# Kernel tuning notes

Hardware: AMD Instinct MI355X
Metric: run time of the kernel (lower is better)

## Reference

```python
import jax, jax.numpy as jnp
import numpy as np

ALPHA = 0.15  # top-k fraction (forward default)


def setup_inputs() -> dict:
    key = jax.random.key(0)
    k1, k2, k3 = jax.random.split(key, 3)
    B, N, D = 8, 1024, 256
    x = jax.random.normal(k1, (B, N, D), dtype=jnp.float32)
    # torch nn.Linear(dim, H*head_dim, bias=False); stored here as [D, H*head_dim]
    W_src = jax.random.normal(k2, (D, D), dtype=jnp.float32) * (1.0 / np.sqrt(D))
    W_tgt = jax.random.normal(k3, (D, D), dtype=jnp.float32) * (1.0 / np.sqrt(D))
    return {"x": x, "W_src": W_src, "W_tgt": W_tgt}


def _topk_mask(adj, k):
    # adj: [B,H,N,N]; exact scatter of 1.0 at top-k indices along last axis
    B, H, N, _ = adj.shape
    _, idx = jax.lax.top_k(adj, k)              # [B,H,N,k]
    bi = jnp.arange(B)[:, None, None, None]
    hi = jnp.arange(H)[None, :, None, None]
    ni = jnp.arange(N)[None, None, :, None]
    mask = jnp.zeros_like(adj).at[bi, hi, ni, idx].set(1.0)
    return mask


def reference(x, W_src, W_tgt):
    # directed=True path of DirectedGraphLearner.forward
    B, N, D = x.shape
    H, head_dim = 4, D // 4
    k = max(1, int(ALPHA * N))
    src = (x @ W_src).reshape(B, N, H, head_dim)
    tgt = (x @ W_tgt).reshape(B, N, H, head_dim)
    adj = jnp.einsum('bihd,bjhd->bhij', src, tgt)
    adj = jax.nn.gelu(adj, approximate=False)    # torch F.gelu default = exact erf
    mask = _topk_mask(adj, k)
    return adj * mask
```

## Files before the change

kernel.cpp:

```cpp
#include <hip/hip_runtime.h>
#include <math.h>


#define KSEL 153u
#define EPSK 61000u

typedef __attribute__((ext_vector_type(8))) short short8v;
typedef __attribute__((ext_vector_type(4))) float float4v;

__device__ __forceinline__ float gelu_f32(float x) {
    return 0.5f * x * (1.0f + erff(x * 0.70710678118654752f));
}

__device__ __forceinline__ unsigned long long d2key(double v) {
    unsigned long long u = (unsigned long long)__double_as_longlong(v);
    return (u >> 63) ? ~u : (u | 0x8000000000000000ull);
}

__device__ __forceinline__ unsigned lkeyf(float v) {
    float q = fmaf(v, 33554432.0f, 2147483648.0f);
    q = fminf(fmaxf(q, 0.0f), 4294967040.0f);
    return (unsigned)q;
}

__device__ __forceinline__ unsigned short b16(float x) {
    unsigned u = __float_as_uint(x);
    u += 0x7FFFu + ((u >> 16) & 1u);
    return (unsigned short)(u >> 16);
}
__device__ __forceinline__ float bf2f(unsigned short h) {
    return __uint_as_float(((unsigned)h) << 16);
}
__device__ __forceinline__ unsigned pk2(float a, float b) {
    return (unsigned)b16(a) | ((unsigned)b16(b) << 16);
}

#define LGKM0()                                             \
    do {                                                    \
        asm volatile("s_waitcnt lgkmcnt(0)" ::: "memory");  \
        __builtin_amdgcn_sched_barrier(0);                  \
    } while (0)

template <bool W32>
__global__ __launch_bounds__(256) void k1_proj(const float* __restrict__ x,
                                               const float* __restrict__ Wsrc,
                                               const float* __restrict__ Wtgt,
                                               double* __restrict__ ws,
                                               unsigned short* __restrict__ th,
                                               unsigned short* __restrict__ tl) {
    __shared__ float xs[32 * 68];
    __shared__ float wsh[32 * 68];
    const int t = threadIdx.x;
    const int bx = blockIdx.x;
    const int by = blockIdx.y;
    const int col0 = (by & 3) * 64;
    const float* __restrict__ W = (by < 4) ? Wsrc : Wtgt;
    double* __restrict__ outp = ws + ((by < 4) ? 0 : 2097152);

    double acc[4][4];
#pragma unroll
    for (int i = 0; i < 4; ++i)
#pragma unroll
        for (int j = 0; j < 4; ++j) acc[i][j] = 0.0;

    const int m_loc = (t & 15) * 4;
    const int c_loc = (t >> 4) * 4;

    for (int kt = 0; kt < 8; ++kt) {
        __syncthreads();
#pragma unroll
        for (int it = 0; it < 2; ++it) {
            int f4 = t + 256 * it;
            int m = f4 >> 3, k4 = f4 & 7;
            float4 v = *reinterpret_cast<const float4*>(&x[(bx * 64 + m) * 256 + kt * 32 + 4 * k4]);
            xs[(4 * k4 + 0) * 68 + m] = v.x;
            xs[(4 * k4 + 1) * 68 + m] = v.y;
            xs[(4 * k4 + 2) * 68 + m] = v.z;
            xs[(4 * k4 + 3) * 68 + m] = v.w;
        }
#pragma unroll
        for (int it = 0; it < 2; ++it) {
            int f4 = t + 256 * it;
            int k = f4 >> 4, c4 = f4 & 15;
            *reinterpret_cast<float4*>(&wsh[k * 68 + 4 * c4]) =
                *reinterpret_cast<const float4*>(&W[(kt * 32 + k) * 256 + col0 + 4 * c4]);
        }
        __syncthreads();
#pragma unroll
        for (int kk = 0; kk < 32; ++kk) {
            float4 a = *reinterpret_cast<const float4*>(&xs[kk * 68 + m_loc]);
            float4 b = *reinterpret_cast<const float4*>(&wsh[kk * 68 + c_loc]);
            double ad[4] = {a.x, a.y, a.z, a.w};
            double bd[4] = {b.x, b.y, b.z, b.w};
#pragma unroll
            for (int i = 0; i < 4; ++i)
#pragma unroll
                for (int j = 0; j < 4; ++j) acc[i][j] += ad[i] * bd[j];
        }
    }
    const int hd = by & 3;
#pragma unroll
    for (int i = 0; i < 4; ++i) {
        int m = bx * 64 + m_loc + i;
        int b = m >> 10, n = m & 1023;
        int bhd = b * 4 + hd;
        size_t base = ((size_t)(bhd * 1024 + n)) * 64 + c_loc;
        double2 v01, v23;
        v01.x = acc[i][0]; v01.y = acc[i][1];
        v23.x = acc[i][2]; v23.y = acc[i][3];
        *reinterpret_cast<double2*>(&outp[base]) = v01;
        *reinterpret_cast<double2*>(&outp[base + 2]) = v23;
        if (W32 && by >= 4) {
            float f0 = (float)acc[i][0], f1 = (float)acc[i][1];
            float f2 = (float)acc[i][2], f3 = (float)acc[i][3];
            unsigned short h0 = b16(f0), h1 = b16(f1), h2 = b16(f2), h3 = b16(f3);
            uint2 H, L;
            H.x = (unsigned)h0 | ((unsigned)h1 << 16);
            H.y = (unsigned)h2 | ((unsigned)h3 << 16);
            L.x = pk2(f0 - bf2f(h0), f1 - bf2f(h1));
            L.y = pk2(f2 - bf2f(h2), f3 - bf2f(h3));
            *reinterpret_cast<uint2*>(&th[base]) = H;
            *reinterpret_cast<uint2*>(&tl[base]) = L;
        }
    }
}

template <bool FAST>
__global__ __launch_bounds__(256, 4) void k2_fused(const double* __restrict__ srcT,
                                                   const double* __restrict__ tgtT,
                                                   const unsigned short* __restrict__ th,
                                                   const unsigned short* __restrict__ tlo,
                                                   float* __restrict__ out) {
    __shared__ float tr[16 * 512];
    __shared__ unsigned short srcf[2][1024];
    __shared__ __align__(16) unsigned hist[4][256];

    const int t = threadIdx.x;
    const int lane = t & 63;
    const int wv = t >> 6;
    const int bid = (blockIdx.x & 7) * 256 + (blockIdx.x >> 3);
    const int bh = bid >> 6;
    const int itile = bid & 63;
    const int row0 = itile * 16;
    const int r0 = 4 * wv;
    const size_t tgtBase = (size_t)bh * 65536;
    const unsigned short* __restrict__ thb = th + tgtBase;
    const unsigned short* __restrict__ tlb = tlo + tgtBase;

    {
        int r = t >> 4, dq = (t & 15) * 4;
        const double* sp = &srcT[((size_t)bh * 1024 + row0 + r) * 64 + dq];
        double2 a = *reinterpret_cast<const double2*>(sp);
        double2 b = *reinterpret_cast<const double2*>(sp + 2);
        float f0 = (float)a.x, f1 = (float)a.y, f2 = (float)b.x, f3 = (float)b.y;
        unsigned short h0 = b16(f0), h1 = b16(f1), h2 = b16(f2), h3 = b16(f3);
        int s = dq >> 3;
        int idx = r * 64 + ((s ^ (r & 7)) << 3) + (dq & 7);
        uint2 H, L;
        H.x = (unsigned)h0 | ((unsigned)h1 << 16);
        H.y = (unsigned)h2 | ((unsigned)h3 << 16);
        L.x = pk2(f0 - bf2f(h0), f1 - bf2f(h1));
        L.y = pk2(f2 - bf2f(h2), f3 - bf2f(h3));
        *reinterpret_cast<uint2*>(&srcf[0][idx]) = H;
        *reinterpret_cast<uint2*>(&srcf[1][idx]) = L;
    }
    __syncthreads();

    short8v Ah[2], Al[2];
#pragma unroll
    for (int ks = 0; ks < 2; ++ks) {
        int idxA = (lane & 15) * 64 + (((4 * ks + (lane >> 4)) ^ (lane & 7)) << 3);
        Ah[ks] = *reinterpret_cast<const short8v*>(&srcf[0][idxA]);
        Al[ks] = *reinterpret_cast<const short8v*>(&srcf[1][idxA]);
    }

    const int colA = lane & 15;
    const int kgrp = lane >> 4;
    float vals[4][16];

#pragma unroll
    for (int h = 0; h < 2; ++h) {
        float4v acc[8];
#pragma unroll
        for (int a = 0; a < 8; ++a) acc[a] = (float4v){0.f, 0.f, 0.f, 0.f};

#pragma unroll
        for (int u = 0; u < 8; ++u) {
            const int T = 32 * h + 4 * u + wv;
            const size_t cbase = (size_t)(16 * T + colA) * 64 + kgrp * 8;
#pragma unroll
            for (int ks = 0; ks < 2; ++ks) {
                short8v Bh, Bl;
                if (FAST) {
                    Bh = *reinterpret_cast<const short8v*>(&thb[cbase + 32 * ks]);
                    Bl = *reinterpret_cast<const short8v*>(&tlb[cbase + 32 * ks]);
                } else {
                    const double* gp = &tgtT[tgtBase + cbase + 32 * ks];
                    double2 d0 = *reinterpret_cast<const double2*>(gp);
                    double2 d1 = *reinterpret_cast<const double2*>(gp + 2);
                    double2 d2 = *reinterpret_cast<const double2*>(gp + 4);
                    double2 d3 = *reinterpret_cast<const double2*>(gp + 6);
                    float f[8] = {(float)d0.x, (float)d0.y, (float)d1.x, (float)d1.y,
                                  (float)d2.x, (float)d2.y, (float)d3.x, (float)d3.y};
                    unsigned short hh[8];
#pragma unroll
                    for (int e = 0; e < 8; ++e) hh[e] = b16(f[e]);
                    unsigned Hw[4], Lw[4];
#pragma unroll
                    for (int e = 0; e < 4; ++e) {
                        Hw[e] = (unsigned)hh[2 * e] | ((unsigned)hh[2 * e + 1] << 16);
                        Lw[e] = pk2(f[2 * e] - bf2f(hh[2 * e]), f[2 * e + 1] - bf2f(hh[2 * e + 1]));
                    }
                    Bh = *reinterpret_cast<const short8v*>(Hw);
                    Bl = *reinterpret_cast<const short8v*>(Lw);
                }
                acc[u] = __builtin_amdgcn_mfma_f32_16x16x32_bf16(Ah[ks], Bh, acc[u], 0, 0, 0);
                acc[u] = __builtin_amdgcn_mfma_f32_16x16x32_bf16(Al[ks], Bh, acc[u], 0, 0, 0);
                acc[u] = __builtin_amdgcn_mfma_f32_16x16x32_bf16(Ah[ks], Bl, acc[u], 0, 0, 0);
            }
        }

        __syncthreads();
#pragma unroll
        for (int u = 0; u < 8; ++u) {
            int colh = 16 * (4 * u + wv) + colA;
#pragma unroll
            for (int reg = 0; reg < 4; ++reg) {
                int row = 4 * kgrp + reg;
                tr[row * 512 + (colh ^ ((row & 1) << 4))] = acc[u][reg];
            }
        }
        __syncthreads();
#pragma unroll
        for (int ri = 0; ri < 4; ++ri) {
            int row = r0 + ri;
#pragma unroll
            for (int mm = 0; mm < 8; ++mm) {
                int colh = lane + 64 * mm;
                vals[ri][8 * h + mm] = tr[row * 512 + (colh ^ ((row & 1) << 4))];
            }
        }
    }

    const size_t outBase = ((size_t)bh * 1024 + row0 + r0) * 1024;
    unsigned* cjp = &hist[wv][128];
    unsigned long long* ckp = reinterpret_cast<unsigned long long*>(&hist[wv][0]);
    unsigned* ccp = &hist[wv][192];

#pragma unroll
    for (int ri = 0; ri < 4; ++ri) {
        unsigned ul[16];
#pragma unroll
        for (int m = 0; m < 16; ++m) ul[m] = lkeyf(vals[ri][m]);

        unsigned prefA = 0u, maskA = 0u, rk = KSEL;
#pragma unroll 1
        for (int p = 1; p >= 0; --p) {
            const int sh = 16 + 8 * p;
            *reinterpret_cast<uint4*>(&hist[wv][4 * lane]) = make_uint4(0u, 0u, 0u, 0u);
            LGKM0();
#pragma unroll
            for (int m = 0; m < 16; ++m) {
                if ((ul[m] & maskA) == prefA)
                    atomicAdd(&hist[wv][(ul[m] >> sh) & 255u], 1u);
            }
            LGKM0();
            unsigned h0 = hist[wv][4 * lane + 0], h1 = hist[wv][4 * lane + 1];
            unsigned h2 = hist[wv][4 * lane + 2], h3 = hist[wv][4 * lane + 3];
            unsigned S = h0 + h1 + h2 + h3;
            unsigned inc = S;
#pragma unroll
            for (int off = 1; off < 64; off <<= 1) {
                unsigned o = __shfl_down(inc, off, 64);
                inc = (lane + off < 64) ? (inc + o) : inc;
            }
            unsigned above = inc - S;
            bool found = (above < rk) && (rk <= inc);
            unsigned long long bal = __ballot(found);
            int L = __ffsll(bal) - 1;
            unsigned hh[4];
            hh[0] = __shfl(h0, L, 64);
            hh[1] = __shfl(h1, L, 64);
            hh[2] = __shfl(h2, L, 64);
            hh[3] = __shfl(h3, L, 64);
            unsigned cum = __shfl(above, L, 64);
            int bsel = -1;
#pragma unroll
            for (int q = 3; q >= 0; --q) {
                if (bsel < 0) {
                    if (rk <= cum + hh[q]) {
                        bsel = q;
                        rk = rk - cum;
                    } else {
                        cum += hh[q];
                    }
                }
            }
            prefA |= (unsigned)(4 * L + bsel) << sh;
            maskA |= 0xFFu << sh;
        }

        const unsigned klo = prefA - EPSK;
        const unsigned khi = prefA + 65535u + EPSK;

        int ch = 0, cb = 0;
#pragma unroll
        for (int m = 0; m < 16; ++m) {
            ch += (ul[m] > khi) ? 1 : 0;
            cb += (ul[m] >= klo && ul[m] <= khi) ? 1 : 0;
        }
#pragma unroll
        for (int off = 32; off; off >>= 1) {
            ch += __shfl_xor(ch, off, 64);
            cb += __shfl_xor(cb, off, 64);
        }
        const unsigned need = KSEL - (unsigned)ch;
        const bool fastp = ((unsigned)cb == need);

        unsigned long long selMask = 0ull;
        unsigned cidx[16];
        if (!fastp) {
            if (lane == 0) *ccp = 0u;
            LGKM0();
#pragma unroll
            for (int m = 0; m < 16; ++m) {
                cidx[m] = 0xFFFFFFFFu;
                if (ul[m] >= klo && ul[m] <= khi) {
                    unsigned idx = atomicAdd(ccp, 1u);
                    cidx[m] = idx;
                    if (idx < 64u) cjp[idx] = (unsigned)(lane + 64 * m);
                }
            }
            LGKM0();
            unsigned g = *ccp;
            if (g > 64u) g = 64u;
            unsigned rnk = need;
            if (lane < (int)g) {
                unsigned j = cjp[lane];
                const double2* sp = reinterpret_cast<const double2*>(
                    &srcT[((size_t)bh * 1024 + row0 + r0 + ri) * 64]);
                const double2* tp = reinterpret_cast<const double2*>(&tgtT[tgtBase + (size_t)j * 64]);
                double a2 = 0.0;
#pragma unroll 8
                for (int d2 = 0; d2 < 32; ++d2) {
                    double2 aa = sp[d2], bb = tp[d2];
                    a2 = fma(aa.x, bb.x, fma(aa.y, bb.y, a2));
                }
                ckp[lane] = d2key(a2);
            }
            LGKM0();
            if (lane < (int)g) {
                unsigned long long myk = ckp[lane];
                unsigned myj = cjp[lane];
                rnk = 0;
                for (unsigned i = 0; i < g; ++i) {
                    unsigned long long ki = ckp[i];
                    rnk += (ki > myk || (ki == myk && cjp[i] < myj)) ? 1u : 0u;
                }
            }
            selMask = __ballot(lane < (int)g && rnk < need);
        }

        const size_t rowBase = outBase + (size_t)ri * 1024;
#pragma unroll
        for (int m = 0; m < 16; ++m) {
            bool sel;
            if (ul[m] > khi) sel = true;
            else if (ul[m] < klo) sel = false;
            else sel = fastp ? true
                             : ((cidx[m] < 64u) ? (((selMask >> cidx[m]) & 1ull) != 0ull) : false);
            float v = vals[ri][m];
            float g = 0.0f;
            if (sel) g = (v > 3.0f) ? v : gelu_f32(v);
            out[rowBase + (unsigned)(lane + 64 * m)] = g;
        }
    }
}

extern "C" void kernel_launch(void* const* d_in, const int* in_sizes, int n_in,
                              void* d_out, int out_size, void* d_ws, size_t ws_size,
                              hipStream_t stream) {
    const float* x = (const float*)d_in[0];
    const float* Wsrc = (const float*)d_in[1];
    const float* Wtgt = (const float*)d_in[2];
    float* out = (float*)d_out;
    double* ws = (double*)d_ws;
    unsigned short* th = (unsigned short*)((char*)d_ws + 33554432);
    unsigned short* tl = (unsigned short*)((char*)d_ws + 37748736);

    const bool fast = (ws_size >= 40u * 1024u * 1024u);
    dim3 g1(128, 8);
    if (fast) {
        k1_proj<true><<<g1, 256, 0, stream>>>(x, Wsrc, Wtgt, ws, th, tl);
        k2_fused<true><<<2048, 256, 0, stream>>>(ws, ws + 2097152, th, tl, out);
    } else {
        k1_proj<false><<<g1, 256, 0, stream>>>(x, Wsrc, Wtgt, ws, th, tl);
        k2_fused<false><<<2048, 256, 0, stream>>>(ws, ws + 2097152, th, tl, out);
    }
}
```

Before: 184.1 us.

## Double-buffer B fragment loads and batch radix-select across four rows

In the fast path, the B operand fragments for the next column tile are loaded into a two-slot register buffer while the MFMAs for the current tile run, hiding load latency. The per-row radix select is restructured so all four rows of a wave build histograms together in the reused transpose buffer, with their prefix scans and shuffles interleaved. This raises instruction-level parallelism and removes per-row serialization. The cost is more register pressure, keys recomputed instead of cached, and an extra block barrier.

```diff
diff --git a/kernel.cpp b/kernel.cpp
--- a/kernel.cpp
+++ b/kernel.cpp
@@ -184,17 +184,40 @@
 #pragma unroll
         for (int a = 0; a < 8; ++a) acc[a] = (float4v){0.f, 0.f, 0.f, 0.f};
 
+        short8v pBh[2][2], pBl[2][2];
+        if (FAST) {
+            const size_t cb0 = (size_t)(16 * (32 * h + wv) + colA) * 64 + kgrp * 8;
+#pragma unroll
+            for (int ks = 0; ks < 2; ++ks) {
+                pBh[0][ks] = *reinterpret_cast<const short8v*>(&thb[cb0 + 32 * ks]);
+                pBl[0][ks] = *reinterpret_cast<const short8v*>(&tlb[cb0 + 32 * ks]);
+            }
+        }
+
 #pragma unroll
         for (int u = 0; u < 8; ++u) {
-            const int T = 32 * h + 4 * u + wv;
-            const size_t cbase = (size_t)(16 * T + colA) * 64 + kgrp * 8;
-#pragma unroll
-            for (int ks = 0; ks < 2; ++ks) {
-                short8v Bh, Bl;
-                if (FAST) {
-                    Bh = *reinterpret_cast<const short8v*>(&thb[cbase + 32 * ks]);
-                    Bl = *reinterpret_cast<const short8v*>(&tlb[cbase + 32 * ks]);
-                } else {
+            if (FAST) {
+                const int pu = u & 1;
+                if (u < 7) {
+                    const size_t cb2 =
+                        (size_t)(16 * (32 * h + 4 * (u + 1) + wv) + colA) * 64 + kgrp * 8;
+#pragma unroll
+                    for (int ks = 0; ks < 2; ++ks) {
+                        pBh[pu ^ 1][ks] = *reinterpret_cast<const short8v*>(&thb[cb2 + 32 * ks]);
+                        pBl[pu ^ 1][ks] = *reinterpret_cast<const short8v*>(&tlb[cb2 + 32 * ks]);
+                    }
+                }
+#pragma unroll
+                for (int ks = 0; ks < 2; ++ks) {
+                    acc[u] = __builtin_amdgcn_mfma_f32_16x16x32_bf16(Ah[ks], pBh[pu][ks], acc[u], 0, 0, 0);
+                    acc[u] = __builtin_amdgcn_mfma_f32_16x16x32_bf16(Al[ks], pBh[pu][ks], acc[u], 0, 0, 0);
+                    acc[u] = __builtin_amdgcn_mfma_f32_16x16x32_bf16(Ah[ks], pBl[pu][ks], acc[u], 0, 0, 0);
+                }
+            } else {
+                const int T = 32 * h + 4 * u + wv;
+                const size_t cbase = (size_t)(16 * T + colA) * 64 + kgrp * 8;
+#pragma unroll
+                for (int ks = 0; ks < 2; ++ks) {
                     const double* gp = &tgtT[tgtBase + cbase + 32 * ks];
                     double2 d0 = *reinterpret_cast<const double2*>(gp);
                     double2 d1 = *reinterpret_cast<const double2*>(gp + 2);
@@ -211,12 +234,12 @@
                         Hw[e] = (unsigned)hh[2 * e] | ((unsigned)hh[2 * e + 1] << 16);
                         Lw[e] = pk2(f[2 * e] - bf2f(hh[2 * e]), f[2 * e + 1] - bf2f(hh[2 * e + 1]));
                     }
-                    Bh = *reinterpret_cast<const short8v*>(Hw);
-                    Bl = *reinterpret_cast<const short8v*>(Lw);
-                }
-                acc[u] = __builtin_amdgcn_mfma_f32_16x16x32_bf16(Ah[ks], Bh, acc[u], 0, 0, 0);
-                acc[u] = __builtin_amdgcn_mfma_f32_16x16x32_bf16(Al[ks], Bh, acc[u], 0, 0, 0);
-                acc[u] = __builtin_amdgcn_mfma_f32_16x16x32_bf16(Ah[ks], Bl, acc[u], 0, 0, 0);
+                    short8v Bh = *reinterpret_cast<const short8v*>(Hw);
+                    short8v Bl = *reinterpret_cast<const short8v*>(Lw);
+                    acc[u] = __builtin_amdgcn_mfma_f32_16x16x32_bf16(Ah[ks], Bh, acc[u], 0, 0, 0);
+                    acc[u] = __builtin_amdgcn_mfma_f32_16x16x32_bf16(Al[ks], Bh, acc[u], 0, 0, 0);
+                    acc[u] = __builtin_amdgcn_mfma_f32_16x16x32_bf16(Ah[ks], Bl, acc[u], 0, 0, 0);
+                }
             }
         }
 
@@ -242,49 +265,62 @@
         }
     }
 
-    const size_t outBase = ((size_t)bh * 1024 + row0 + r0) * 1024;
-    unsigned* cjp = &hist[wv][128];
-    unsigned long long* ckp = reinterpret_cast<unsigned long long*>(&hist[wv][0]);
-    unsigned* ccp = &hist[wv][192];
-
-#pragma unroll
-    for (int ri = 0; ri < 4; ++ri) {
-        unsigned ul[16];
-#pragma unroll
-        for (int m = 0; m < 16; ++m) ul[m] = lkeyf(vals[ri][m]);
-
-        unsigned prefA = 0u, maskA = 0u, rk = KSEL;
+    __syncthreads();
+
+    unsigned (*hx)[256] = reinterpret_cast<unsigned (*)[256]>(tr);
+
+    unsigned pref[4] = {0u, 0u, 0u, 0u};
+    unsigned rkk[4] = {KSEL, KSEL, KSEL, KSEL};
+
 #pragma unroll 1
-        for (int p = 1; p >= 0; --p) {
-            const int sh = 16 + 8 * p;
-            *reinterpret_cast<uint4*>(&hist[wv][4 * lane]) = make_uint4(0u, 0u, 0u, 0u);
-            LGKM0();
+    for (int p = 1; p >= 0; --p) {
+        const int sh = 16 + 8 * p;
+        const unsigned mA = (p == 1) ? 0u : 0xFF000000u;
+
+#pragma unroll
+        for (int ri = 0; ri < 4; ++ri)
+            *reinterpret_cast<uint4*>(&hx[4 * wv + ri][4 * lane]) = make_uint4(0u, 0u, 0u, 0u);
+        LGKM0();
+#pragma unroll
+        for (int ri = 0; ri < 4; ++ri)
 #pragma unroll
             for (int m = 0; m < 16; ++m) {
-                if ((ul[m] & maskA) == prefA)
-                    atomicAdd(&hist[wv][(ul[m] >> sh) & 255u], 1u);
-            }
-            LGKM0();
-            unsigned h0 = hist[wv][4 * lane + 0], h1 = hist[wv][4 * lane + 1];
-            unsigned h2 = hist[wv][4 * lane + 2], h3 = hist[wv][4 * lane + 3];
-            unsigned S = h0 + h1 + h2 + h3;
-            unsigned inc = S;
-#pragma unroll
-            for (int off = 1; off < 64; off <<= 1) {
-                unsigned o = __shfl_down(inc, off, 64);
-                inc = (lane + off < 64) ? (inc + o) : inc;
-            }
-            unsigned above = inc - S;
-            bool found = (above < rk) && (rk <= inc);
+                unsigned key = lkeyf(vals[ri][m]);
+                if ((key & mA) == (pref[ri] & mA))
+                    atomicAdd(&hx[4 * wv + ri][(key >> sh) & 255u], 1u);
+            }
+        LGKM0();
+
+        unsigned h0[4], h1[4], h2[4], h3[4], S[4], inc[4];
+#pragma unroll
+        for (int ri = 0; ri < 4; ++ri) {
+            uint4 hv = *reinterpret_cast<const uint4*>(&hx[4 * wv + ri][4 * lane]);
+            h0[ri] = hv.x; h1[ri] = hv.y; h2[ri] = hv.z; h3[ri] = hv.w;
+            S[ri] = hv.x + hv.y + hv.z + hv.w;
+            inc[ri] = S[ri];
+        }
+#pragma unroll
+        for (int off = 1; off < 64; off <<= 1) {
+#pragma unroll
+            for (int ri = 0; ri < 4; ++ri) {
+                unsigned o = __shfl_down(inc[ri], off, 64);
+                inc[ri] = (lane + off < 64) ? (inc[ri] + o) : inc[ri];
+            }
+        }
+#pragma unroll
+        for (int ri = 0; ri < 4; ++ri) {
+            unsigned above = inc[ri] - S[ri];
+            bool found = (above < rkk[ri]) && (rkk[ri] <= inc[ri]);
             unsigned long long bal = __ballot(found);
             int L = __ffsll(bal) - 1;
             unsigned hh[4];
-            hh[0] = __shfl(h0, L, 64);
-            hh[1] = __shfl(h1, L, 64);
-            hh[2] = __shfl(h2, L, 64);
-            hh[3] = __shfl(h3, L, 64);
+            hh[0] = __shfl(h0[ri], L, 64);
+            hh[1] = __shfl(h1[ri], L, 64);
+            hh[2] = __shfl(h2[ri], L, 64);
+            hh[3] = __shfl(h3[ri], L, 64);
             unsigned cum = __shfl(above, L, 64);
             int bsel = -1;
+            unsigned rk = rkk[ri];
 #pragma unroll
             for (int q = 3; q >= 0; --q) {
                 if (bsel < 0) {
@@ -296,26 +332,43 @@
                     }
                 }
             }
-            prefA |= (unsigned)(4 * L + bsel) << sh;
-            maskA |= 0xFFu << sh;
-        }
-
-        const unsigned klo = prefA - EPSK;
-        const unsigned khi = prefA + 65535u + EPSK;
-
-        int ch = 0, cb = 0;
+            rkk[ri] = rk;
+            pref[ri] |= (unsigned)(4 * L + bsel) << sh;
+        }
+    }
+
+    unsigned klo[4], khi[4];
+    int ch[4], cb[4];
+#pragma unroll
+    for (int ri = 0; ri < 4; ++ri) {
+        klo[ri] = pref[ri] - EPSK;
+        khi[ri] = pref[ri] + 65535u + EPSK;
+        ch[ri] = 0; cb[ri] = 0;
 #pragma unroll
         for (int m = 0; m < 16; ++m) {
-            ch += (ul[m] > khi) ? 1 : 0;
-            cb += (ul[m] >= klo && ul[m] <= khi) ? 1 : 0;
-        }
-#pragma unroll
-        for (int off = 32; off; off >>= 1) {
-            ch += __shfl_xor(ch, off, 64);
-            cb += __shfl_xor(cb, off, 64);
-        }
-        const unsigned need = KSEL - (unsigned)ch;
-        const bool fastp = ((unsigned)cb == need);
+            unsigned key = lkeyf(vals[ri][m]);
+            ch[ri] += (key > khi[ri]) ? 1 : 0;
+            cb[ri] += (key >= klo[ri] && key <= khi[ri]) ? 1 : 0;
+        }
+    }
+#pragma unroll
+    for (int off = 32; off; off >>= 1) {
+#pragma unroll
+        for (int ri = 0; ri < 4; ++ri) {
+            ch[ri] += __shfl_xor(ch[ri], off, 64);
+            cb[ri] += __shfl_xor(cb[ri], off, 64);
+        }
+    }
+
+    const size_t outBase = ((size_t)bh * 1024 + row0 + r0) * 1024;
+    unsigned* cjp = &hist[wv][128];
+    unsigned long long* ckp = reinterpret_cast<unsigned long long*>(&hist[wv][0]);
+    unsigned* ccp = &hist[wv][192];
+
+#pragma unroll
+    for (int ri = 0; ri < 4; ++ri) {
+        const unsigned need = KSEL - (unsigned)ch[ri];
+        const bool fastp = ((unsigned)cb[ri] == need);
 
         unsigned long long selMask = 0ull;
         unsigned cidx[16];
@@ -325,7 +378,8 @@
 #pragma unroll
             for (int m = 0; m < 16; ++m) {
                 cidx[m] = 0xFFFFFFFFu;
-                if (ul[m] >= klo && ul[m] <= khi) {
+                unsigned key = lkeyf(vals[ri][m]);
+                if (key >= klo[ri] && key <= khi[ri]) {
                     unsigned idx = atomicAdd(ccp, 1u);
                     cidx[m] = idx;
                     if (idx < 64u) cjp[idx] = (unsigned)(lane + 64 * m);
@@ -364,9 +418,10 @@
         const size_t rowBase = outBase + (size_t)ri * 1024;
 #pragma unroll
         for (int m = 0; m < 16; ++m) {
+            unsigned key = lkeyf(vals[ri][m]);
             bool sel;
-            if (ul[m] > khi) sel = true;
-            else if (ul[m] < klo) sel = false;
+            if (key > khi[ri]) sel = true;
+            else if (key < klo[ri]) sel = false;
             else sel = fastp ? true
                              : ((cidx[m] < 64u) ? (((selMask >> cidx[m]) & 1ull) != 0ull) : false);
             float v = vals[ri][m];
```

Result: slower. 229.6 us (+24.7%).
